# Kernel tuning notes

Measured on AMD Instinct MI355X. Metric: run time of the kernel, lower is better.

Reference implementation:

```python
import jax, jax.numpy as jnp
import numpy as np

B, N, D_MODEL, H, DK, DV = 8, 512, 512, 8, 64, 64
MAX_DIST = 512
NUM_REL = 2 * MAX_DIST - 1  # 1023


def setup_inputs() -> dict:
    key = jax.random.key(0)
    ks = jax.random.split(key, 12)
    s = 0.02
    return {
        "X": jax.random.normal(ks[0], (B, N, D_MODEL), jnp.float32),
        "Wq": jax.random.normal(ks[1], (D_MODEL, H * DK), jnp.float32) * s,
        "bq": jnp.zeros((H * DK,), jnp.float32),
        "Wk": jax.random.normal(ks[2], (D_MODEL, H * DK), jnp.float32) * s,
        "bk": jnp.zeros((H * DK,), jnp.float32),
        "Wv": jax.random.normal(ks[3], (D_MODEL, H * DV), jnp.float32) * s,
        "bv": jnp.zeros((H * DV,), jnp.float32),
        "Wo": jax.random.normal(ks[4], (H * DV, D_MODEL), jnp.float32) * s,
        "bo": jnp.zeros((D_MODEL,), jnp.float32),
        "P_k": jax.random.normal(ks[5], (NUM_REL, H), jnp.float32),
        "P_v": jax.random.normal(ks[6], (NUM_REL, H, DV), jnp.float32),
    }


def reference(X, Wq, bq, Wk, bk, Wv, bv, Wo, bo, P_k, P_v):
    b, n, d = X.shape
    scale = 1.0 / jnp.sqrt(jnp.float32(DK))
    # projections -> [b, h, n, d]
    Q = (X @ Wq + bq).reshape(b, n, H, DK).transpose(0, 2, 1, 3)
    K = (X @ Wk + bk).reshape(b, n, H, DK).transpose(0, 2, 1, 3)
    V = (X @ Wv + bv).reshape(b, n, H, DV).transpose(0, 2, 1, 3)
    # relative index: rel[i, j] = zero_offset + (j - i)
    zero_offset = NUM_REL // 2
    rel = zero_offset + (jnp.arange(n)[None, :] - jnp.arange(n)[:, None])  # [n, n]
    A_k = P_k[rel]  # [n, n, h]
    scores = (jnp.einsum("bhid,bhjd->bhij", Q, K) + A_k.transpose(2, 0, 1)[None]) * scale
    attn = jax.nn.softmax(scores, axis=-1)  # [b, h, n, n]
    # standard value mixing + relative value mixing (einsum avoids the
    # explicit [b,h,n,n,dv] broadcast the torch code materializes; same math)
    A_v = P_v[rel]  # [n, n, h, dv]
    out = jnp.einsum("bhij,bhjd->bhid", attn, V) + jnp.einsum("bhij,ijhd->bhid", attn, A_v)
    out = out.transpose(0, 2, 1, 3).reshape(b, n, H * DV)
    return out @ Wo + bo
```

## Files before the change

kernel.cpp:

```cpp
#include <hip/hip_runtime.h>
#include <math.h>

#define Bc 8
#define Nseq 512
#define DM 512
#define Hh 8
#define NUMREL 1023
#define ZOFF 511
#define STR 552

typedef _Float16 half8 __attribute__((ext_vector_type(8)));
typedef float f32x4 __attribute__((ext_vector_type(4)));

__device__ __forceinline__ unsigned short f2h(float f) {
  _Float16 h = (_Float16)f;
  return __builtin_bit_cast(unsigned short, h);
}

typedef __attribute__((address_space(3))) unsigned int as3_uint;
typedef __attribute__((address_space(1))) const unsigned int as1_uint;
__device__ __forceinline__ void gl_lds16(const void* g, void* l) {
  __builtin_amdgcn_global_load_lds((as1_uint*)g, (as3_uint*)l, 16, 0, 0);
}

__global__ __launch_bounds__(256) void prep_all(
    const float* __restrict__ X, const float* __restrict__ Wq,
    const float* __restrict__ Wk, const float* __restrict__ Wv,
    const float* __restrict__ Wo, const float* __restrict__ Pk,
    const float* __restrict__ Pv,
    unsigned short* __restrict__ XbF, unsigned short* __restrict__ WqF,
    unsigned short* __restrict__ WkF, unsigned short* __restrict__ WvF,
    unsigned short* __restrict__ WoF,
    float* __restrict__ Pkt, unsigned short* __restrict__ PvF2) {
  __shared__ float tbuf[5120];
  const int bid = blockIdx.x;
  const int tid = threadIdx.x;

  if (bid < 1024) {
    const int w = tid >> 6, lane = tid & 63;
    const int r = bid * 4 + w;
    const float* src = X + (size_t)r * DM + lane * 8;
    float4 a = *(const float4*)src;
    float4 b = *(const float4*)(src + 4);
    ushort4 o0, o1;
    o0.x = f2h(a.x); o0.y = f2h(a.y); o0.z = f2h(a.z); o0.w = f2h(a.w);
    o1.x = f2h(b.x); o1.y = f2h(b.y); o1.z = f2h(b.z); o1.w = f2h(b.w);
    const int mc = r >> 4, kf = lane >> 2, l = (lane & 3) * 16 + (r & 15);
    size_t flat = (((size_t)mc * 16 + kf) * 64 + l) * 8;
    *(ushort4*)(XbF + flat) = o0;
    *(ushort4*)(XbF + flat + 4) = o1;
  } else if (bid < 2048) {
    const int idx = bid - 1024;
    const int z = idx >> 8, r256 = idx & 255;
    const int bx = r256 & 15, by = r256 >> 4;
    const float* src = z == 0 ? Wq : z == 1 ? Wk : z == 2 ? Wv : Wo;
    unsigned short* dst = z == 0 ? WqF : z == 1 ? WkF : z == 2 ? WvF : WoF;
    const int k0 = by * 32, n0 = bx * 32;
#pragma unroll
    for (int u = 0; u < 4; ++u) {
      int i2 = u * 256 + tid, r = i2 >> 5, c = i2 & 31;
      tbuf[r * 33 + c] = src[(size_t)(k0 + r) * DM + n0 + c];
    }
    __syncthreads();
    const int ncl = tid >> 7, l = (tid >> 1) & 63, eh = tid & 1;
    const int nl = ncl * 16 + (l & 15);
    const int klb = (l >> 4) * 8 + eh * 4;
    ushort4 o;
    o.x = f2h(tbuf[(klb + 0) * 33 + nl]);
    o.y = f2h(tbuf[(klb + 1) * 33 + nl]);
    o.z = f2h(tbuf[(klb + 2) * 33 + nl]);
    o.w = f2h(tbuf[(klb + 3) * 33 + nl]);
    size_t flat = (((size_t)((n0 >> 4) + ncl) * 16 + (k0 >> 5)) * 64 + l) * 8 + eh * 4;
    *(ushort4*)(dst + flat) = o;
  } else if (bid < 2088) {
    const int idx = bid - 2048;
    const int gx = idx % 5, h = idx / 5;
    const int g = gx * 256 + tid;
    if (g < 1040)
      Pkt[(size_t)h * 1040 + g] = (g < NUMREL) ? Pk[(size_t)g * Hh + h] : 0.f;
  } else {
    const int idx = bid - 2088;
    const int gx = idx & 15, h = idx >> 4;
    const int g0 = gx * 64;
#pragma unroll
    for (int u = 0; u < 20; ++u) {
      int i2 = u * 256 + tid, r = i2 >> 6, c = i2 & 63;
      int g = g0 + r;
      tbuf[r * 64 + c] = (g < NUMREL) ? Pv[(size_t)g * 512 + h * 64 + c] : 0.f;
    }
    __syncthreads();
#pragma unroll
    for (int av = 0; av < 2; ++av)
#pragma unroll
      for (int gtl = 0; gtl < 2; ++gtl) {
        int gt = (g0 >> 5) + gtl;
#pragma unroll
        for (int dt = 0; dt < 4; ++dt) {
          size_t base = ((((size_t)av * Hh + h) * 4 + dt) * 32 + gt) * 512;
          int i2 = tid * 2;
          int l = i2 >> 3, e = i2 & 7;
          int gr = av * 16 + gtl * 32 + (l >> 4) * 8 + e;
          int dcol = dt * 16 + (l & 15);
          ushort2 o;
          o.x = f2h(tbuf[gr * 64 + dcol]);
          o.y = f2h(tbuf[(gr + 1) * 64 + dcol]);
          *(ushort2*)(PvF2 + base + i2) = o;
        }
      }
  }
}

__global__ __launch_bounds__(256, 2) void gemm_qkv(const unsigned short* __restrict__ XbF,
                                                   const unsigned short* __restrict__ WqF,
                                                   const unsigned short* __restrict__ WkF,
                                                   const unsigned short* __restrict__ WvF,
                                                   const float* __restrict__ bq,
                                                   const float* __restrict__ bk,
                                                   const float* __restrict__ bv,
                                                   unsigned short* __restrict__ Qb,
                                                   unsigned short* __restrict__ KF,
                                                   unsigned short* __restrict__ VF) {
  const int flat = blockIdx.x;
  const int xcd = flat & 7, g = flat >> 3;
  const int by = xcd * 8 + (g & 7), bx = g >> 3;
  const int bm = by * 64, bn = bx * 64;
  const int mc0 = bm >> 4, nc0 = bn >> 4;
  const int tid = threadIdx.x, w = tid >> 6, lane = tid & 63;
  const int lo = lane & 15, quad = lane >> 4;
  const int mh = (w >> 1) * 2, nh = (w & 1) * 2;

  __shared__ __align__(16) unsigned short stg[2][32 * 512];

  const unsigned short* srcArr = w == 0 ? XbF : w == 1 ? WqF : w == 2 ? WkF : WvF;
  const int rowbase = (w == 0) ? mc0 : nc0;

#define STAGE(buf, ks)                                                             \
  do {                                                                             \
    _Pragma("unroll") for (int t = 0; t < 8; ++t) {                                \
      gl_lds16(srcArr +                                                            \
                   (((size_t)(rowbase + (t >> 1)) * 16 + 2 * (ks) + (t & 1)) * 512) + \
                   lane * 8,                                                       \
               &stg[buf][(w * 8 + t) * 512]);                                      \
    }                                                                              \
  } while (0)

  f32x4 acc[3][2][2] = {};
  STAGE(0, 0);
  int cur = 0;
#pragma unroll
  for (int ks = 0; ks < 8; ++ks) {
    __syncthreads();
    if (ks < 7) STAGE(cur ^ 1, ks + 1);
#pragma unroll
    for (int kf = 0; kf < 2; ++kf) {
      half8 af[2], bq_[2], bk_[2], bv_[2];
#pragma unroll
      for (int i = 0; i < 2; ++i)
        af[i] = *(const half8*)(&stg[cur][((mh + i) * 2 + kf) * 512 + lane * 8]);
#pragma unroll
      for (int j = 0; j < 2; ++j) {
        bq_[j] = *(const half8*)(&stg[cur][(8 + (nh + j) * 2 + kf) * 512 + lane * 8]);
        bk_[j] = *(const half8*)(&stg[cur][(16 + (nh + j) * 2 + kf) * 512 + lane * 8]);
        bv_[j] = *(const half8*)(&stg[cur][(24 + (nh + j) * 2 + kf) * 512 + lane * 8]);
      }
#pragma unroll
      for (int i = 0; i < 2; ++i)
#pragma unroll
        for (int j = 0; j < 2; ++j) {
          acc[0][i][j] = __builtin_amdgcn_mfma_f32_16x16x32_f16(af[i], bq_[j], acc[0][i][j], 0, 0, 0);
          acc[1][i][j] = __builtin_amdgcn_mfma_f32_16x16x32_f16(af[i], bk_[j], acc[1][i][j], 0, 0, 0);
          acc[2][i][j] = __builtin_amdgcn_mfma_f32_16x16x32_f16(af[i], bv_[j], acc[2][i][j], 0, 0, 0);
        }
    }
    cur ^= 1;
  }
#undef STAGE

  const int mt = (w >> 1) * 32, nt = (w & 1) * 32;
#pragma unroll
  for (int z = 0; z < 3; ++z) {
    const float* bias = z == 0 ? bq : z == 1 ? bk : bv;
#pragma unroll
    for (int i = 0; i < 2; ++i)
#pragma unroll
      for (int j = 0; j < 2; ++j) {
        int col = bn + nt + j * 16 + lo;
        int h = col >> 6, d = col & 63;
        float bb = bias[col];
#pragma unroll
        for (int r = 0; r < 4; ++r) {
          int row = bm + mt + i * 16 + quad * 4 + r;
          int b = row >> 9, is = row & 511;
          int bh = b * Hh + h;
          unsigned short val = f2h(acc[z][i][j][r] + bb);
          if (z == 0) {
            Qb[((size_t)bh * Nseq + is) * 64 + d] = val;
          } else if (z == 1) {
            int jt = is >> 4, kf2 = d >> 5, l = ((d >> 3) & 3) * 16 + (is & 15), e = d & 7;
            KF[(((size_t)bh * 32 + jt) * 2 + kf2) * 512 + l * 8 + e] = val;
          } else {
            int dt = d >> 4, ks = is >> 5, l = ((is >> 3) & 3) * 16 + (d & 15), e = is & 7;
            VF[(((size_t)bh * 4 + dt) * 16 + ks) * 512 + l * 8 + e] = val;
          }
        }
      }
  }
}

__global__ __launch_bounds__(256, 3) void attn_fused(
    const unsigned short* __restrict__ Qb,
    const unsigned short* __restrict__ KF,
    const unsigned short* __restrict__ VF,
    const float* __restrict__ Pkt,
    const unsigned short* __restrict__ PvF2,
    unsigned short* __restrict__ AwF) {
  const int flat = blockIdx.x;
  const int h = flat & 7;
  const int grp = flat >> 3;
  const int b = grp >> 4;
  const int p = grp & 15;
  const int itA = (p >> 1) * 4 + (p & 1);
  const int i0A = itA * 16;
  const int bh = b * Hh + h;
  const int tid = threadIdx.x, w = tid >> 6, lane = tid & 63;
  const int lo = lane & 15, quad = lane >> 4;

  __shared__ __align__(16) unsigned short pstA[16 * STR];
  __shared__ __align__(16) unsigned short pstB[16 * STR];
  __shared__ float pk_lds[560];
  __shared__ float redm[128];
  __shared__ float redl[128];

  const int TB = 464 - i0A;

  int4 z4; z4.x = z4.y = z4.z = z4.w = 0;
  for (int c = tid; c < 16 * STR / 8; c += 256) {
    ((int4*)pstA)[c] = z4;
    ((int4*)pstB)[c] = z4;
  }
  for (int c = tid; c < 140; c += 256)
    *(float4*)(pk_lds + c * 4) = *(const float4*)(Pkt + (size_t)h * 1040 + TB + c * 4);

  const unsigned short* qA = Qb + ((size_t)bh * Nseq + i0A + lo) * 64;
  const unsigned short* qB = Qb + ((size_t)bh * Nseq + i0A + 32 + lo) * 64;
  half8 qa0 = *(const half8*)(qA + quad * 8);
  half8 qa1 = *(const half8*)(qA + 32 + quad * 8);
  half8 qb0 = *(const half8*)(qB + quad * 8);
  half8 qb1 = *(const half8*)(qB + 32 + quad * 8);

  const unsigned short* KFb = KF + ((size_t)bh * 64 + (size_t)w * 16) * 512 + lane * 8;
  const unsigned short* VFb = VF + ((size_t)bh * 4 + w) * 16 * 512 + lane * 8;
  const int aP = (TB >> 4) & 1, gtB = TB >> 5;
  const unsigned short* PFb =
      PvF2 + ((((size_t)aP * Hh + h) * 4 + w) * 32 + gtB) * 512 + lane * 8;

  __syncthreads();

  float svA[8][4], svB[8][4];
  float mA[4] = {-1e30f, -1e30f, -1e30f, -1e30f};
  float mB[4] = {-1e30f, -1e30f, -1e30f, -1e30f};
#pragma unroll
  for (int g = 0; g < 8; ++g) {
    half8 k0 = *(const half8*)(KFb + (size_t)(2 * g + 0) * 512);
    half8 k1 = *(const half8*)(KFb + (size_t)(2 * g + 1) * 512);
    f32x4 cA = {0.f, 0.f, 0.f, 0.f};
    f32x4 cB = {0.f, 0.f, 0.f, 0.f};
    cA = __builtin_amdgcn_mfma_f32_16x16x32_f16(qa0, k0, cA, 0, 0, 0);
    cA = __builtin_amdgcn_mfma_f32_16x16x32_f16(qa1, k1, cA, 0, 0, 0);
    cB = __builtin_amdgcn_mfma_f32_16x16x32_f16(qb0, k0, cB, 0, 0, 0);
    cB = __builtin_amdgcn_mfma_f32_16x16x32_f16(qb1, k1, cB, 0, 0, 0);
    int j = w * 128 + g * 16 + lo;
#pragma unroll
    for (int r = 0; r < 4; ++r) {
      int rl = quad * 4 + r;
      int idx = j - rl + 15;
      float vA = (cA[r] + pk_lds[idx + 32]) * 0.125f;
      float vB = (cB[r] + pk_lds[idx]) * 0.125f;
      svA[g][r] = vA; svB[g][r] = vB;
      mA[r] = fmaxf(mA[r], vA);
      mB[r] = fmaxf(mB[r], vB);
    }
  }

#pragma unroll
  for (int m = 1; m <= 8; m <<= 1)
#pragma unroll
    for (int r = 0; r < 4; ++r) {
      mA[r] = fmaxf(mA[r], __shfl_xor(mA[r], m));
      mB[r] = fmaxf(mB[r], __shfl_xor(mB[r], m));
    }
  if (lo == 0)
#pragma unroll
    for (int r = 0; r < 4; ++r) {
      redm[(0 * 4 + w) * 16 + quad * 4 + r] = mA[r];
      redm[(1 * 4 + w) * 16 + quad * 4 + r] = mB[r];
    }
  __syncthreads();
  float mfA[4], mfB[4];
#pragma unroll
  for (int r = 0; r < 4; ++r) {
    int rl = quad * 4 + r;
    mfA[r] = fmaxf(fmaxf(redm[rl], redm[16 + rl]), fmaxf(redm[32 + rl], redm[48 + rl]));
    mfB[r] = fmaxf(fmaxf(redm[64 + rl], redm[80 + rl]), fmaxf(redm[96 + rl], redm[112 + rl]));
  }
  float lA[4] = {0.f, 0.f, 0.f, 0.f}, lB[4] = {0.f, 0.f, 0.f, 0.f};
#pragma unroll
  for (int s = 0; s < 8; ++s)
#pragma unroll
    for (int r = 0; r < 4; ++r) {
      float eA = __expf(svA[s][r] - mfA[r]);
      float eB = __expf(svB[s][r] - mfB[r]);
      svA[s][r] = eA; svB[s][r] = eB;
      lA[r] += eA; lB[r] += eB;
    }
#pragma unroll
  for (int m = 1; m <= 8; m <<= 1)
#pragma unroll
    for (int r = 0; r < 4; ++r) {
      lA[r] += __shfl_xor(lA[r], m);
      lB[r] += __shfl_xor(lB[r], m);
    }
  if (lo == 0)
#pragma unroll
    for (int r = 0; r < 4; ++r) {
      redl[(0 * 4 + w) * 16 + quad * 4 + r] = lA[r];
      redl[(1 * 4 + w) * 16 + quad * 4 + r] = lB[r];
    }
  __syncthreads();
  float liA[4], liB[4];
#pragma unroll
  for (int r = 0; r < 4; ++r) {
    int rl = quad * 4 + r;
    liA[r] = 1.f / (redl[rl] + redl[16 + rl] + redl[32 + rl] + redl[48 + rl]);
    liB[r] = 1.f / (redl[64 + rl] + redl[80 + rl] + redl[96 + rl] + redl[112 + rl]);
#pragma unroll
    for (int s = 0; s < 8; ++s) {
      int j = w * 128 + s * 16 + lo;
      pstA[rl * STR + 16 + j] = f2h(svA[s][r]);
      pstB[rl * STR + 16 + j] = f2h(svB[s][r]);
    }
  }
  __syncthreads();

  f32x4 oVA = {0.f, 0.f, 0.f, 0.f}, oVB = {0.f, 0.f, 0.f, 0.f};
#pragma unroll
  for (int g = 0; g < 8; ++g) {
    half8 v0 = *(const half8*)(VFb + (size_t)(2 * g + 0) * 512);
    half8 v1 = *(const half8*)(VFb + (size_t)(2 * g + 1) * 512);
#pragma unroll
    for (int c = 0; c < 2; ++c) {
      int ks = 2 * g + c;
      half8 vv = c ? v1 : v0;
      half8 pA = *(const half8*)(&pstA[lo * STR + 16 + ks * 32 + quad * 8]);
      half8 pB = *(const half8*)(&pstB[lo * STR + 16 + ks * 32 + quad * 8]);
      oVA = __builtin_amdgcn_mfma_f32_16x16x32_f16(pA, vv, oVA, 0, 0, 0);
      oVB = __builtin_amdgcn_mfma_f32_16x16x32_f16(pB, vv, oVB, 0, 0, 0);
    }
  }

  f32x4 oPA = {0.f, 0.f, 0.f, 0.f}, oPB = {0.f, 0.f, 0.f, 0.f};
#pragma unroll
  for (int g = 0; g < 9; ++g) {
    half8 p0 = *(const half8*)(PFb + (size_t)(2 * g + 0) * 512);
    half8 p1 = *(const half8*)(PFb + (size_t)(2 * g + 1) * 512);
#pragma unroll
    for (int c = 0; c < 2; ++c) {
      int cg = 2 * g + c;
      half8 pvf = c ? p1 : p0;
      if (cg < 17) {
        union { half8 v; unsigned short s8[8]; } pa;
        if (cg == 16 && quad >= 2) {
#pragma unroll
          for (int e = 0; e < 8; ++e) pa.s8[e] = 0;
        } else {
          int base = lo * STR + cg * 32 + quad * 8 + lo + 1;
#pragma unroll
          for (int e = 0; e < 8; ++e) pa.s8[e] = pstB[base + e];
        }
        oPB = __builtin_amdgcn_mfma_f32_16x16x32_f16(pa.v, pvf, oPB, 0, 0, 0);
      }
      if (cg >= 1) {
        int ksA = cg - 1;
        union { half8 v; unsigned short s8[8]; } pa;
        if (ksA == 16 && quad >= 2) {
#pragma unroll
          for (int e = 0; e < 8; ++e) pa.s8[e] = 0;
        } else {
          int base = lo * STR + ksA * 32 + quad * 8 + lo + 1;
#pragma unroll
          for (int e = 0; e < 8; ++e) pa.s8[e] = pstA[base + e];
        }
        oPA = __builtin_amdgcn_mfma_f32_16x16x32_f16(pa.v, pvf, oPA, 0, 0, 0);
      }
    }
  }

  const int kf = h * 2 + (w >> 1);
  const int lhi = ((w & 1) * 2 + (lo >> 3)) * 16;
#pragma unroll
  for (int t = 0; t < 2; ++t) {
    int mc = b * 32 + itA + t * 2;
#pragma unroll
    for (int r = 0; r < 4; ++r) {
      float ov = t ? (oVB[r] + oPB[r]) * liB[r] : (oVA[r] + oPA[r]) * liA[r];
      size_t fl = (((size_t)mc * 16 + kf) * 64 + lhi + quad * 4 + r) * 8 + (lo & 7);
      AwF[fl] = f2h(ov);
    }
  }
}

__global__ __launch_bounds__(256, 2) void gemm_final(const unsigned short* __restrict__ AF,
                                                     const unsigned short* __restrict__ BF,
                                                     const float* __restrict__ bo,
                                                     float* __restrict__ out) {
  const int flat = blockIdx.x;
  const int xcd = flat & 7, g = flat >> 3;
  const int by = xcd * 8 + (g & 7), bx = g >> 3;
  const int bm = by * 64, bn = bx * 64;
  const int mc0 = bm >> 4, nc0 = bn >> 4;
  const int tid = threadIdx.x, w = tid >> 6, lane = tid & 63;
  const int lo = lane & 15, quad = lane >> 4;
  const int mh = (w >> 1) * 2, nh = (w & 1) * 2;

  __shared__ __align__(16) unsigned short stg[2][16 * 512];

  const unsigned short* srcArr = (w < 2) ? AF : BF;
  const int rowbase = ((w < 2) ? mc0 : nc0) + (w & 1) * 2;

#define STAGE2(buf, ks)                                                            \
  do {                                                                             \
    _Pragma("unroll") for (int t = 0; t < 4; ++t) {                                \
      gl_lds16(srcArr +                                                            \
                   (((size_t)(rowbase + (t >> 1)) * 16 + 2 * (ks) + (t & 1)) * 512) + \
                   lane * 8,                                                       \
               &stg[buf][(w * 4 + t) * 512]);                                      \
    }                                                                              \
  } while (0)

  f32x4 acc[2][2] = {};
  STAGE2(0, 0);
  int cur = 0;
#pragma unroll
  for (int ks = 0; ks < 8; ++ks) {
    __syncthreads();
    if (ks < 7) STAGE2(cur ^ 1, ks + 1);
#pragma unroll
    for (int kf = 0; kf < 2; ++kf) {
      half8 af[2], bf[2];
#pragma unroll
      for (int i = 0; i < 2; ++i)
        af[i] = *(const half8*)(&stg[cur][((mh + i) * 2 + kf) * 512 + lane * 8]);
#pragma unroll
      for (int j = 0; j < 2; ++j)
        bf[j] = *(const half8*)(&stg[cur][(8 + (nh + j) * 2 + kf) * 512 + lane * 8]);
#pragma unroll
      for (int i = 0; i < 2; ++i)
#pragma unroll
        for (int j = 0; j < 2; ++j)
          acc[i][j] = __builtin_amdgcn_mfma_f32_16x16x32_f16(af[i], bf[j], acc[i][j], 0, 0, 0);
    }
    cur ^= 1;
  }
#undef STAGE2

  const int mt = (w >> 1) * 32, nt = (w & 1) * 32;
#pragma unroll
  for (int i = 0; i < 2; ++i)
#pragma unroll
    for (int j = 0; j < 2; ++j) {
      int col = bn + nt + j * 16 + lo;
      float bb = bo[col];
#pragma unroll
      for (int r = 0; r < 4; ++r) {
        int row = bm + mt + i * 16 + quad * 4 + r;
        out[(size_t)row * DM + col] = acc[i][j][r] + bb;
      }
    }
}

extern "C" void kernel_launch(void* const* d_in, const int* in_sizes, int n_in,
                              void* d_out, int out_size, void* d_ws, size_t ws_size,
                              hipStream_t stream) {
  const float* X  = (const float*)d_in[0];
  const float* Wq = (const float*)d_in[1];
  const float* bq = (const float*)d_in[2];
  const float* Wk = (const float*)d_in[3];
  const float* bk = (const float*)d_in[4];
  const float* Wv = (const float*)d_in[5];
  const float* bv = (const float*)d_in[6];
  const float* Wo = (const float*)d_in[7];
  const float* bo = (const float*)d_in[8];
  const float* Pk = (const float*)d_in[9];
  const float* Pv = (const float*)d_in[10];
  float* out = (float*)d_out;

  char* p = (char*)d_ws;
  const size_t szX    = (size_t)Bc * Nseq * DM * 2;
  const size_t szW    = (size_t)DM * DM * 2;
  const size_t szPkt  = (size_t)Hh * 1040 * 4;
  const size_t szPvF2 = (size_t)2 * Hh * 4 * 32 * 512 * 2;
  const size_t szQKV  = (size_t)Bc * Hh * Nseq * 64 * 2;
  unsigned short* XbF = (unsigned short*)p; p += szX;
  unsigned short* WqF = (unsigned short*)p; p += szW;
  unsigned short* WkF = (unsigned short*)p; p += szW;
  unsigned short* WvF = (unsigned short*)p; p += szW;
  unsigned short* WoF = (unsigned short*)p; p += szW;
  float*          Pkt = (float*)p;          p += (szPkt + 255) & ~(size_t)255;
  unsigned short* PvF2 = (unsigned short*)p; p += szPvF2;
  unsigned short* Qb  = (unsigned short*)p; p += szQKV;
  unsigned short* KF  = (unsigned short*)p; p += szQKV;
  unsigned short* VF  = (unsigned short*)p; p += szQKV;
  unsigned short* AwF = (unsigned short*)p; p += szX;

  dim3 blk(256);
  prep_all<<<dim3(2216), blk, 0, stream>>>(X, Wq, Wk, Wv, Wo, Pk, Pv,
                                           XbF, WqF, WkF, WvF, WoF, Pkt, PvF2);
  gemm_qkv<<<dim3(512), blk, 0, stream>>>(XbF, WqF, WkF, WvF, bq, bk, bv, Qb, KF, VF);
  attn_fused<<<dim3(1024), blk, 0, stream>>>(Qb, KF, VF, Pkt, PvF2, AwF);
  gemm_final<<<dim3(512), blk, 0, stream>>>(AwF, WoF, bo, out);
}
```

Before: 137.0 us.

## Store skewed probability copy in LDS to enable vector reads in relative-value MFMA

After the V mixing, the softmax probabilities are rewritten into LDS in a diagonally skewed layout, with an extra overflow region for the tail. The relative-position MFMA loop can then read aligned half8 vectors instead of gathering eight scalar shorts per fragment. Probabilities are packed as fp16 pairs in registers to cut register use, and launch bounds are raised from 3 to 4 blocks per SM. The cost is an extra pass of LDS writes, two more barriers, larger LDS buffers, and possible register spills under the tighter occupancy bound.

Measured after the change: 131.2 us. 1.04x faster.

```diff
diff --git a/kernel.cpp b/kernel.cpp
--- a/kernel.cpp
+++ b/kernel.cpp
@@ -207,7 +207,7 @@
   }
 }
 
-__global__ __launch_bounds__(256, 3) void attn_fused(
+__global__ __launch_bounds__(256, 4) void attn_fused(
     const unsigned short* __restrict__ Qb,
     const unsigned short* __restrict__ KF,
     const unsigned short* __restrict__ VF,
@@ -225,8 +225,8 @@
   const int tid = threadIdx.x, w = tid >> 6, lane = tid & 63;
   const int lo = lane & 15, quad = lane >> 4;
 
-  __shared__ __align__(16) unsigned short pstA[16 * STR];
-  __shared__ __align__(16) unsigned short pstB[16 * STR];
+  __shared__ __align__(16) unsigned short pstA[16 * STR + 512];
+  __shared__ __align__(16) unsigned short pstB[16 * STR + 512];
   __shared__ float pk_lds[560];
   __shared__ float redm[128];
   __shared__ float redl[128];
@@ -234,7 +234,7 @@
   const int TB = 464 - i0A;
 
   int4 z4; z4.x = z4.y = z4.z = z4.w = 0;
-  for (int c = tid; c < 16 * STR / 8; c += 256) {
+  for (int c = tid; c < (16 * STR + 512) / 8; c += 256) {
     ((int4*)pstA)[c] = z4;
     ((int4*)pstB)[c] = z4;
   }
@@ -304,14 +304,15 @@
     mfB[r] = fmaxf(fmaxf(redm[64 + rl], redm[80 + rl]), fmaxf(redm[96 + rl], redm[112 + rl]));
   }
   float lA[4] = {0.f, 0.f, 0.f, 0.f}, lB[4] = {0.f, 0.f, 0.f, 0.f};
+  unsigned int svp[8][4];
 #pragma unroll
   for (int s = 0; s < 8; ++s)
 #pragma unroll
     for (int r = 0; r < 4; ++r) {
       float eA = __expf(svA[s][r] - mfA[r]);
       float eB = __expf(svB[s][r] - mfB[r]);
-      svA[s][r] = eA; svB[s][r] = eB;
       lA[r] += eA; lB[r] += eB;
+      svp[s][r] = (unsigned int)f2h(eA) | ((unsigned int)f2h(eB) << 16);
     }
 #pragma unroll
   for (int m = 1; m <= 8; m <<= 1)
@@ -336,8 +337,8 @@
 #pragma unroll
     for (int s = 0; s < 8; ++s) {
       int j = w * 128 + s * 16 + lo;
-      pstA[rl * STR + 16 + j] = f2h(svA[s][r]);
-      pstB[rl * STR + 16 + j] = f2h(svB[s][r]);
+      pstA[rl * STR + 16 + j] = (unsigned short)svp[s][r];
+      pstB[rl * STR + 16 + j] = (unsigned short)(svp[s][r] >> 16);
     }
   }
   __syncthreads();
@@ -357,6 +358,27 @@
       oVB = __builtin_amdgcn_mfma_f32_16x16x32_f16(pB, vv, oVB, 0, 0, 0);
     }
   }
+  __syncthreads();
+
+#pragma unroll
+  for (int r = 0; r < 4; ++r) {
+    int rl = quad * 4 + r;
+#pragma unroll
+    for (int s = 0; s < 8; ++s) {
+      int j = w * 128 + s * 16 + lo;
+      int x = j - rl + 15;
+      unsigned int pv = svp[s][r];
+      if (w == 3 && s == 7) {
+        int addr = (x < 512) ? (rl * STR + x) : (16 * STR + rl * 32 + (x - 512));
+        pstA[addr] = (unsigned short)pv;
+        pstB[addr] = (unsigned short)(pv >> 16);
+      } else {
+        pstA[rl * STR + x] = (unsigned short)pv;
+        pstB[rl * STR + x] = (unsigned short)(pv >> 16);
+      }
+    }
+  }
+  __syncthreads();
 
   f32x4 oPA = {0.f, 0.f, 0.f, 0.f}, oPB = {0.f, 0.f, 0.f, 0.f};
 #pragma unroll
@@ -368,29 +390,17 @@
       int cg = 2 * g + c;
       half8 pvf = c ? p1 : p0;
       if (cg < 17) {
-        union { half8 v; unsigned short s8[8]; } pa;
-        if (cg == 16 && quad >= 2) {
-#pragma unroll
-          for (int e = 0; e < 8; ++e) pa.s8[e] = 0;
-        } else {
-          int base = lo * STR + cg * 32 + quad * 8 + lo + 1;
-#pragma unroll
-          for (int e = 0; e < 8; ++e) pa.s8[e] = pstB[base + e];
-        }
-        oPB = __builtin_amdgcn_mfma_f32_16x16x32_f16(pa.v, pvf, oPB, 0, 0, 0);
+        const unsigned short* src = (cg < 16)
+            ? &pstB[lo * STR + cg * 32 + quad * 8]
+            : &pstB[16 * STR + lo * 32 + quad * 8];
+        oPB = __builtin_amdgcn_mfma_f32_16x16x32_f16(*(const half8*)src, pvf, oPB, 0, 0, 0);
       }
       if (cg >= 1) {
         int ksA = cg - 1;
-        union { half8 v; unsigned short s8[8]; } pa;
-        if (ksA == 16 && quad >= 2) {
-#pragma unroll
-          for (int e = 0; e < 8; ++e) pa.s8[e] = 0;
-        } else {
-          int base = lo * STR + ksA * 32 + quad * 8 + lo + 1;
-#pragma unroll
-          for (int e = 0; e < 8; ++e) pa.s8[e] = pstA[base + e];
-        }
-        oPA = __builtin_amdgcn_mfma_f32_16x16x32_f16(pa.v, pvf, oPA, 0, 0, 0);
+        const unsigned short* src = (ksA < 16)
+            ? &pstA[lo * STR + ksA * 32 + quad * 8]
+            : &pstA[16 * STR + lo * 32 + quad * 8];
+        oPA = __builtin_amdgcn_mfma_f32_16x16x32_f16(*(const half8*)src, pvf, oPA, 0, 0, 0);
       }
     }
   }
```
